# Optimization experiments

Measured on AMD Instinct MI355X. Metric: run time of the kernel, lower is better.

Reference implementation:

```python
import jax, jax.numpy as jnp
import numpy as np


def maxpool2x2(x):
    # NCHW 2x2 max pool, stride 2
    return jax.lax.reduce_window(x, -jnp.inf, jax.lax.max, (1, 1, 2, 2), (1, 1, 2, 2), 'VALID')


def _xavier_uniform(k, shape):
    fan_out, fan_in = shape
    lim = np.sqrt(6.0 / (fan_in + fan_out))
    return jax.random.uniform(k, shape, jnp.float32, -lim, lim)


def setup_inputs() -> dict:
    key = jax.random.key(0)
    ks = jax.random.split(key, 5)
    C = 64
    x = jax.random.normal(ks[0], (4, C, 128, 128), jnp.float32)
    Wq = _xavier_uniform(ks[1], (C // 8, C))  # 1x1 conv == channel matmul
    Wk = _xavier_uniform(ks[2], (C // 8, C))
    Wv = _xavier_uniform(ks[3], (C // 2, C))
    Wo = _xavier_uniform(ks[4], (C, C // 2))
    gamma = jnp.full((1,), 0.1, jnp.float32)  # nonzero so attention branch contributes
    return {"x": x, "Wq": Wq, "Wk": Wk, "Wv": Wv, "Wo": Wo, "gamma": gamma}


def reference(x, Wq, Wk, Wv, Wo, gamma):
    b, c, w, h = x.shape
    # 1x1 convs as channel contractions
    q = jnp.einsum('oc,bchw->bohw', Wq, x).reshape(b, c // 8, w * h)          # [b, c/8, k]
    k_ = maxpool2x2(jnp.einsum('oc,bchw->bohw', Wk, x)).reshape(b, c // 8, -1)  # [b, c/8, f]
    v = maxpool2x2(jnp.einsum('oc,bchw->bohw', Wv, x)).reshape(b, c // 2, -1)   # [b, c/2, f]
    # softmax over full-resolution query positions k (last axis), per pooled position f
    weights = jax.nn.softmax(jnp.einsum('bcf,bck->bfk', k_, q), axis=-1)        # [b, f, k]
    out = jnp.einsum('bcf,bfk->bck', v, weights).reshape(b, c // 2, w, h)       # [b, c/2, w, h]
    out = jnp.einsum('oc,bchw->bohw', Wo, out)                                   # [b, c, w, h]
    return gamma * out + x
```

## Files before the change

kernel.cpp:

```cpp
#include <hip/hip_runtime.h>
#include <cstdint>
#include <cstddef>


#define LOG2E 1.44269504088896340736f
#define FE_A 8388608.0f
#define FE_B 1064993098.0f

typedef __attribute__((ext_vector_type(8)))  __bf16 bf8_t;
typedef __attribute__((ext_vector_type(16))) float  fx16;

__device__ __forceinline__ unsigned short f2bf(float f) {
  unsigned int u = __builtin_bit_cast(unsigned int, f);
  u += 0x7FFFu + ((u >> 16) & 1u);
  return (unsigned short)(u >> 16);
}
__device__ __forceinline__ float bf2f(unsigned short h) {
  unsigned int u = ((unsigned int)h) << 16;
  return __builtin_bit_cast(float, u);
}
__device__ __forceinline__ unsigned int pk2(unsigned short lo, unsigned short hi) {
  return (unsigned int)lo | ((unsigned int)hi << 16);
}
__device__ __forceinline__ int pi16(int s) {
  int m = (s >> 2) & 3;
  return (m == 1 || m == 2) ? (s ^ 12) : s;
}
__device__ __forceinline__ unsigned fe_u(float s) {
  return (unsigned)fmaf(s, FE_A, FE_B);
}
__device__ __forceinline__ float fe_f(float s) {
  return __builtin_bit_cast(float, fe_u(s));
}
__device__ __forceinline__ unsigned fe_pk(float s0, float s1) {
  return __builtin_amdgcn_perm(fe_u(s1), fe_u(s0), 0x07060302);
}

#define MFMA __builtin_amdgcn_mfma_f32_32x32x16_bf16

__global__ void __launch_bounds__(256) k_qkv(const float* __restrict__ x,
                                             const float* __restrict__ Wq,
                                             const float* __restrict__ Wk,
                                             const float* __restrict__ Wv,
                                             const float* __restrict__ Wo,
                                             unsigned short* __restrict__ Qp,
                                             unsigned short* __restrict__ KpB,
                                             float* __restrict__ Vp,
                                             unsigned short* __restrict__ Wop) {
  if (blockIdx.x == 512) {
    for (int i = threadIdx.x; i < 2048; i += 256) {
      int c = i & 31;
      Wop[i] = f2bf(Wo[(i & ~31) | (c & 16) | pi16(c & 15)]);
    }
    return;
  }
  __shared__ unsigned int xs[128 * 64];
  int t = threadIdx.x;
  int b = blockIdx.x >> 7, rr = blockIdx.x & 127;
  int T = rr >> 1, ph = rr & 1;
  {
    int pos = t & 127, cslot = t >> 7;
    int r = pos >> 6, c = pos & 63;
    const float* xb =
        x + (size_t)b * (64 * 16384) + T * 256 + r * 128 + ph * 64 + c;
    int sw = pos & 15;
    unsigned int* row = xs + pos * 64;
#pragma unroll
    for (int i = 0; i < 16; ++i) {
      int p = cslot * 16 + i;
      float g0 = xb[(size_t)(2 * p) * 16384];
      float g1 = xb[(size_t)(2 * p + 1) * 16384];
      unsigned short h0 = f2bf(g0), h1 = f2bf(g1);
      unsigned short l0 = f2bf(g0 - bf2f(h0)), l1 = f2bf(g1 - bf2f(h1));
      int q = p >> 2, d = p & 3;
      row[((q + sw) & 15) * 4 + d] = pk2(h0, h1);
      row[((q + 8 + sw) & 15) * 4 + d] = pk2(l0, l1);
    }
  }
  int wv = t >> 6, lane = t & 63;
  int cg = wv & 1, Mt = wv >> 1;
  int m = lane & 31, h = lane >> 5;
  const float* wrow;
  float scale = 1.0f;
  bool zero = false;
  if (Mt == 0) {
    if (m < 8) wrow = Wq + m * 64;
    else if (m < 16) { wrow = Wk + (m - 8) * 64; scale = LOG2E; }
    else wrow = Wv + (m - 16) * 64;
  } else {
    if (m < 16) wrow = Wv + (m + 16) * 64;
    else { wrow = Wq; zero = true; }
  }
  bf8_t Ahi[4], Alo[4];
#pragma unroll
  for (int kk = 0; kk < 4; ++kk) {
    unsigned short hi8[8], lo8[8];
#pragma unroll
    for (int j = 0; j < 8; ++j) {
      float w = zero ? 0.f : wrow[kk * 16 + h * 8 + j] * scale;
      unsigned short wh = f2bf(w);
      hi8[j] = wh;
      lo8[j] = f2bf(w - bf2f(wh));
    }
    uint4 uh, ul;
    uh.x = pk2(hi8[0], hi8[1]); uh.y = pk2(hi8[2], hi8[3]);
    uh.z = pk2(hi8[4], hi8[5]); uh.w = pk2(hi8[6], hi8[7]);
    ul.x = pk2(lo8[0], lo8[1]); ul.y = pk2(lo8[2], lo8[3]);
    ul.z = pk2(lo8[4], lo8[5]); ul.w = pk2(lo8[6], lo8[7]);
    Ahi[kk] = __builtin_bit_cast(bf8_t, uh);
    Alo[kk] = __builtin_bit_cast(bf8_t, ul);
  }
  __syncthreads();
  fx16 z;
#pragma unroll
  for (int i = 0; i < 16; ++i) z[i] = 0.f;
  fx16 D0 = z, D1 = z;
#pragma unroll
  for (int r = 0; r < 2; ++r) {
    fx16 acc = z;
    int pos = r * 64 + cg * 32 + (lane & 31);
    const unsigned int* row = xs + pos * 64;
    int sw = pos & 15;
#pragma unroll
    for (int kk = 0; kk < 4; ++kk) {
      int q = 2 * kk + h;
      bf8_t Bh = *reinterpret_cast<const bf8_t*>(&row[((q + sw) & 15) * 4]);
      bf8_t Bl = *reinterpret_cast<const bf8_t*>(&row[((q + 8 + sw) & 15) * 4]);
      acc = MFMA(Ahi[kk], Bh, acc, 0, 0, 0);
      acc = MFMA(Ahi[kk], Bl, acc, 0, 0, 0);
      acc = MFMA(Alo[kk], Bh, acc, 0, 0, 0);
    }
    if (r == 0) D0 = acc; else D1 = acc;
  }
  uint2 z2; z2.x = z2.y = 0u;
  if (Mt == 0) {
#pragma unroll
    for (int r = 0; r < 2; ++r) {
      const fx16& D = r ? D1 : D0;
      int gpos = T * 256 + r * 128 + ph * 64 + cg * 32 + (lane & 31);
      unsigned short* qd = Qp + ((size_t)b * 16384 + gpos) * 16;
      uint2 qa;
      qa.x = pk2(f2bf(D[0]), f2bf(D[1]));
      qa.y = pk2(f2bf(D[2]), f2bf(D[3]));
      *reinterpret_cast<uint2*>(qd + h * 4) = qa;
      *reinterpret_cast<uint2*>(qd + 8 + h * 4) = z2;
    }
  }
  float pm[16];
#pragma unroll
  for (int r0 = 0; r0 < 16; ++r0) {
    float a = fmaxf(D0[r0], __shfl_xor(D0[r0], 1));
    float bb = fmaxf(D1[r0], __shfl_xor(D1[r0], 1));
    pm[r0] = fmaxf(a, bb);
  }
  if ((lane & 1) == 0) {
    int cell = ph * 32 + cg * 16 + ((lane & 31) >> 1);
    size_t idx = (size_t)b * 4096 + T * 64 + cell;
    float* vd = Vp + idx * 32;
    if (Mt == 0) {
      uint2 kw;
      kw.x = pk2(f2bf(pm[4]), f2bf(pm[5]));
      kw.y = pk2(f2bf(pm[6]), f2bf(pm[7]));
      *reinterpret_cast<uint2*>(KpB + idx * 16 + h * 4) = kw;
      *reinterpret_cast<float4*>(vd + h * 4) = make_float4(pm[8], pm[9], pm[10], pm[11]);
      *reinterpret_cast<float4*>(vd + 8 + h * 4) = make_float4(pm[12], pm[13], pm[14], pm[15]);
    } else {
      *reinterpret_cast<uint2*>(KpB + idx * 16 + 8 + h * 4) = z2;
      *reinterpret_cast<float4*>(vd + 16 + h * 4) = make_float4(pm[0], pm[1], pm[2], pm[3]);
      *reinterpret_cast<float4*>(vd + 24 + h * 4) = make_float4(pm[4], pm[5], pm[6], pm[7]);
    }
  }
}

__global__ void __launch_bounds__(64, 4) k_lsum(const unsigned short* __restrict__ Qp,
                                                const unsigned short* __restrict__ KpB,
                                                float* __restrict__ Lpart) {
  int b = blockIdx.x >> 10, gp = (blockIdx.x >> 4) & 63, ks = blockIdx.x & 15;
  int lane = threadIdx.x & 63;
  int half = lane >> 5, l31 = lane & 31;
  const unsigned short* kb =
      KpB + ((size_t)(b * 4096 + gp * 64 + l31)) * 16 + half * 8;
  bf8_t A0 = *reinterpret_cast<const bf8_t*>(kb);
  bf8_t A1 = *reinterpret_cast<const bf8_t*>(kb + 32 * 16);
  const unsigned short* qbase = Qp + ((size_t)b * 16384) * 16 + half * 8;
  fx16 z;
#pragma unroll
  for (int i = 0; i < 16; ++i) z[i] = 0.f;
  float l[32];
#pragma unroll
  for (int i = 0; i < 32; ++i) l[i] = 0.f;
  int t0 = ks * 32;
#define QLD(j) (*reinterpret_cast<const bf8_t*>( \
    qbase + (size_t)(((t0 + ((j) & 31)) * 32 + l31)) * 16))
  bf8_t Bc = QLD(0);
  fx16 sp0 = MFMA(A0, Bc, z, 0, 0, 0);
  fx16 sp1 = MFMA(A1, Bc, z, 0, 0, 0);
  Bc = QLD(1);
  bf8_t Bn = QLD(2);
  for (int i = 0; i < 32; ++i) {
    fx16 sn0 = MFMA(A0, Bc, z, 0, 0, 0);
    fx16 sn1 = MFMA(A1, Bc, z, 0, 0, 0);
#pragma unroll
    for (int r0 = 0; r0 < 16; ++r0) l[r0] += fe_f(sp0[r0]);
#pragma unroll
    for (int r0 = 0; r0 < 16; ++r0) l[16 + r0] += fe_f(sp1[r0]);
    sp0 = sn0; sp1 = sn1;
    Bc = Bn;
    Bn = QLD(i + 3);
  }
#undef QLD
#pragma unroll
  for (int r0 = 0; r0 < 32; ++r0)
    for (int d = 1; d < 32; d <<= 1) l[r0] += __shfl_xor(l[r0], d);
  if (l31 == 0) {
    size_t base = (size_t)ks * 16384 + b * 4096 + gp * 64;
#pragma unroll
    for (int r0 = 0; r0 < 16; ++r0) {
      int row = (r0 & 3) + 8 * (r0 >> 2) + 4 * half;
      Lpart[base + row] = l[r0];
      Lpart[base + 32 + row] = l[16 + r0];
    }
  }
}

__global__ void __launch_bounds__(256) k_pack(const float* __restrict__ Vp,
                                              const float* __restrict__ Lpart,
                                              unsigned short* __restrict__ Vpp) {
  int b = blockIdx.x >> 4, f0 = (blockIdx.x & 15) * 256;
  __shared__ unsigned short Tt[32][264];
  int t = threadIdx.x;
  size_t li = (size_t)b * 4096 + f0 + t;
  float L = 0.f;
#pragma unroll
  for (int p = 0; p < 16; ++p) L += Lpart[(size_t)p * 16384 + li];
  float rl = 1.0f / L;
  const float* vp = Vp + li * 32;
  int fl = (t & ~15) | pi16(t & 15);
  for (int c = 0; c < 32; ++c) Tt[c][fl] = f2bf(vp[c] * rl);
  __syncthreads();
  for (int u = t; u < 1024; u += 256) {
    int row = u >> 5, e0 = (u & 31) * 8;
    uint4 val = *reinterpret_cast<const uint4*>(&Tt[row][e0]);
    *reinterpret_cast<uint4*>(Vpp + ((size_t)b * 32 + row) * 4096 + f0 + e0) = val;
  }
}

__global__ void __launch_bounds__(256, 3) k_attn(const unsigned short* __restrict__ Qp,
                                                 const unsigned short* __restrict__ KpB,
                                                 const unsigned short* __restrict__ Vpp,
                                                 const unsigned short* __restrict__ Wop,
                                                 const float* __restrict__ x,
                                                 const float* __restrict__ gamma,
                                                 float* __restrict__ out) {
  int b = blockIdx.x >> 8, kp = blockIdx.x & 255;
  int wv = threadIdx.x >> 6, lane = threadIdx.x & 63;
  int half = lane >> 5, l31 = lane & 31;
  int kbase = kp * 64;
  const unsigned short* qb = Qp + ((size_t)b * 16384 + kbase + l31) * 16 + half * 8;
  bf8_t Bq0 = *reinterpret_cast<const bf8_t*>(qb);
  bf8_t Bq1 = *reinterpret_cast<const bf8_t*>(qb + 32 * 16);
  fx16 z;
#pragma unroll
  for (int i = 0; i < 16; ++i) z[i] = 0.f;
  fx16 acc0 = z, acc1 = z;
  const unsigned short* kpB = KpB + ((size_t)b * 4096 + l31) * 16 + half * 8;
  const unsigned short* vpB = Vpp + ((size_t)(b * 32 + l31)) * 4096 + half * 8;
  int c0 = wv * 32;
#define KLD(j) (*reinterpret_cast<const bf8_t*>(kpB + (size_t)((c0 + ((j) & 31)) * 32) * 16))
#define VLD(j, o) (*reinterpret_cast<const bf8_t*>(vpB + (c0 + ((j) & 31)) * 32 + (o)))
  bf8_t Akc = KLD(0);
  bf8_t Av0c = VLD(0, 0), Av1c = VLD(0, 16);
  fx16 sp0 = MFMA(Akc, Bq0, z, 0, 0, 0);
  fx16 sp1 = MFMA(Akc, Bq1, z, 0, 0, 0);
  Akc = KLD(1);
  bf8_t Av0n = VLD(1, 0), Av1n = VLD(1, 16);
  bf8_t Akin = KLD(2);
  for (int fc = 0; fc < 32; ++fc) {
    fx16 sn0 = MFMA(Akc, Bq0, z, 0, 0, 0);
    uint4 u00, u01;
    u00.x = fe_pk(sp0[0], sp0[1]);   u00.y = fe_pk(sp0[2], sp0[3]);
    u00.z = fe_pk(sp0[4], sp0[5]);   u00.w = fe_pk(sp0[6], sp0[7]);
    u01.x = fe_pk(sp0[8], sp0[9]);   u01.y = fe_pk(sp0[10], sp0[11]);
    u01.z = fe_pk(sp0[12], sp0[13]); u01.w = fe_pk(sp0[14], sp0[15]);
    acc0 = MFMA(Av0c, __builtin_bit_cast(bf8_t, u00), acc0, 0, 0, 0);
    acc0 = MFMA(Av1c, __builtin_bit_cast(bf8_t, u01), acc0, 0, 0, 0);
    fx16 sn1 = MFMA(Akc, Bq1, z, 0, 0, 0);
    uint4 u10, u11;
    u10.x = fe_pk(sp1[0], sp1[1]);   u10.y = fe_pk(sp1[2], sp1[3]);
    u10.z = fe_pk(sp1[4], sp1[5]);   u10.w = fe_pk(sp1[6], sp1[7]);
    u11.x = fe_pk(sp1[8], sp1[9]);   u11.y = fe_pk(sp1[10], sp1[11]);
    u11.z = fe_pk(sp1[12], sp1[13]); u11.w = fe_pk(sp1[14], sp1[15]);
    acc1 = MFMA(Av0c, __builtin_bit_cast(bf8_t, u10), acc1, 0, 0, 0);
    acc1 = MFMA(Av1c, __builtin_bit_cast(bf8_t, u11), acc1, 0, 0, 0);
    sp0 = sn0; sp1 = sn1;
    Akc = Akin; Av0c = Av0n; Av1c = Av1n;
    Akin = KLD(fc + 3);
    Av0n = VLD(fc + 2, 0); Av1n = VLD(fc + 2, 16);
  }
#undef KLD
#undef VLD
  __shared__ float sacc[4][2][4][64][4];
#pragma unroll
  for (int j4 = 0; j4 < 4; ++j4) {
    *reinterpret_cast<float4*>(&sacc[wv][0][j4][lane][0]) =
        make_float4(acc0[4 * j4], acc0[4 * j4 + 1], acc0[4 * j4 + 2], acc0[4 * j4 + 3]);
    *reinterpret_cast<float4*>(&sacc[wv][1][j4][lane][0]) =
        make_float4(acc1[4 * j4], acc1[4 * j4 + 1], acc1[4 * j4 + 2], acc1[4 * j4 + 3]);
  }
  __syncthreads();
  if (wv >= 2) return;
  int kt = wv;
  int k = kbase + kt * 32 + l31;
  const float* xp = x + (size_t)b * 64 * 16384 + k;
  float xv0[16], xv1[16];
#pragma unroll
  for (int r0 = 0; r0 < 16; ++r0) {
    int row = (r0 & 3) + 8 * (r0 >> 2) + 4 * half;
    xv0[r0] = xp[(size_t)row * 16384];
    xv1[r0] = xp[(size_t)(row + 32) * 16384];
  }
  fx16 tot;
#pragma unroll
  for (int j4 = 0; j4 < 4; ++j4) {
    float4 a0 = *reinterpret_cast<const float4*>(&sacc[0][kt][j4][lane][0]);
    float4 a1 = *reinterpret_cast<const float4*>(&sacc[1][kt][j4][lane][0]);
    float4 a2 = *reinterpret_cast<const float4*>(&sacc[2][kt][j4][lane][0]);
    float4 a3 = *reinterpret_cast<const float4*>(&sacc[3][kt][j4][lane][0]);
    tot[4 * j4]     = (a0.x + a1.x) + (a2.x + a3.x);
    tot[4 * j4 + 1] = (a0.y + a1.y) + (a2.y + a3.y);
    tot[4 * j4 + 2] = (a0.z + a1.z) + (a2.z + a3.z);
    tot[4 * j4 + 3] = (a0.w + a1.w) + (a2.w + a3.w);
  }
  bf8_t Ob0, Ob1;
#pragma unroll
  for (int j = 0; j < 8; ++j) { Ob0[j] = (__bf16)tot[j]; Ob1[j] = (__bf16)tot[8 + j]; }
  const unsigned short* wb = Wop + l31 * 32 + half * 8;
  bf8_t Aw00 = *reinterpret_cast<const bf8_t*>(wb);
  bf8_t Aw01 = *reinterpret_cast<const bf8_t*>(wb + 16);
  bf8_t Aw10 = *reinterpret_cast<const bf8_t*>(wb + 1024);
  bf8_t Aw11 = *reinterpret_cast<const bf8_t*>(wb + 1024 + 16);
  fx16 y0 = MFMA(Aw00, Ob0, z, 0, 0, 0);
  y0 = MFMA(Aw01, Ob1, y0, 0, 0, 0);
  fx16 y1 = MFMA(Aw10, Ob0, z, 0, 0, 0);
  y1 = MFMA(Aw11, Ob1, y1, 0, 0, 0);
  float g = gamma[0];
  float* op = out + (size_t)b * 64 * 16384 + k;
#pragma unroll
  for (int r0 = 0; r0 < 16; ++r0) {
    int row = (r0 & 3) + 8 * (r0 >> 2) + 4 * half;
    op[(size_t)row * 16384]        = fmaf(g, y0[r0], xv0[r0]);
    op[(size_t)(row + 32) * 16384] = fmaf(g, y1[r0], xv1[r0]);
  }
}

extern "C" void kernel_launch(void* const* d_in, const int* in_sizes, int n_in,
                              void* d_out, int out_size, void* d_ws, size_t ws_size,
                              hipStream_t stream) {
  const float* x     = (const float*)d_in[0];
  const float* Wq    = (const float*)d_in[1];
  const float* Wk    = (const float*)d_in[2];
  const float* Wv    = (const float*)d_in[3];
  const float* Wo    = (const float*)d_in[4];
  const float* gamma = (const float*)d_in[5];
  float* out = (float*)d_out;
  char* ws = (char*)d_ws;
  unsigned short* Qp    = (unsigned short*)(ws + 0);
  unsigned short* KpB   = (unsigned short*)(ws + 2097152);
  float*          Vp    = (float*)(ws + 2621440);
  unsigned short* Vpp   = (unsigned short*)(ws + 4718592);
  float*          Lpart = (float*)(ws + 5767168);
  unsigned short* Wop   = (unsigned short*)(ws + 6815744);

  k_qkv <<<dim3(513),  dim3(256), 0, stream>>>(x, Wq, Wk, Wv, Wo, Qp, KpB, Vp, Wop);
  k_lsum<<<dim3(4096), dim3(64),  0, stream>>>(Qp, KpB, Lpart);
  k_pack<<<dim3(64),   dim3(256), 0, stream>>>(Vp, Lpart, Vpp);
  k_attn<<<dim3(1024), dim3(256), 0, stream>>>(Qp, KpB, Vpp, Wop, x, gamma, out);
}
```

Before: 157.4 us.

## Repartition lsum and pack kernels, add explicit MFMA/exp interleaving schedules

k_lsum now gives each 64-lane wave one 32-row key tile over a 32-tile query slice, with two waves per block. This doubles the wave count and halves per-wave register state. It unrolls by two with sched_group_barrier hints so MFMA, loads and exp VALU work interleave. k_pack uses 256 smaller blocks with vectorized float4 loads, and k_attn's main loop is unrolled into even/odd halves with similar scheduling hints. The aim is more parallelism and better latency hiding; the risks are the scheduler constraints hurting codegen and Lpart slice indexing needing to stay consistent.

```diff
diff --git a/kernel.cpp b/kernel.cpp
--- a/kernel.cpp
+++ b/kernel.cpp
@@ -9,6 +9,12 @@
 
 typedef __attribute__((ext_vector_type(8)))  __bf16 bf8_t;
 typedef __attribute__((ext_vector_type(16))) float  fx16;
+
+#if __has_builtin(__builtin_amdgcn_sched_group_barrier)
+#define SGB(m, n) __builtin_amdgcn_sched_group_barrier(m, n, 0)
+#else
+#define SGB(m, n)
+#endif
 
 __device__ __forceinline__ unsigned short f2bf(float f) {
   unsigned int u = __builtin_bit_cast(unsigned int, f);
@@ -172,53 +178,53 @@
   }
 }
 
-__global__ void __launch_bounds__(64, 4) k_lsum(const unsigned short* __restrict__ Qp,
-                                                const unsigned short* __restrict__ KpB,
-                                                float* __restrict__ Lpart) {
-  int b = blockIdx.x >> 10, gp = (blockIdx.x >> 4) & 63, ks = blockIdx.x & 15;
-  int lane = threadIdx.x & 63;
+__global__ void __launch_bounds__(128, 4) k_lsum(const unsigned short* __restrict__ Qp,
+                                                 const unsigned short* __restrict__ KpB,
+                                                 float* __restrict__ Lpart) {
+  int b = blockIdx.x >> 10;
+  int r = blockIdx.x & 1023;
+  int fg = r >> 3, ks = r & 7;
+  int wv = threadIdx.x >> 6, lane = threadIdx.x & 63;
   int half = lane >> 5, l31 = lane & 31;
-  const unsigned short* kb =
-      KpB + ((size_t)(b * 4096 + gp * 64 + l31)) * 16 + half * 8;
-  bf8_t A0 = *reinterpret_cast<const bf8_t*>(kb);
-  bf8_t A1 = *reinterpret_cast<const bf8_t*>(kb + 32 * 16);
+  int slice = ks * 2 + wv;
+  bf8_t A = *reinterpret_cast<const bf8_t*>(
+      KpB + ((size_t)(b * 4096 + fg * 32 + l31)) * 16 + half * 8);
   const unsigned short* qbase = Qp + ((size_t)b * 16384) * 16 + half * 8;
   fx16 z;
 #pragma unroll
   for (int i = 0; i < 16; ++i) z[i] = 0.f;
-  float l[32];
-#pragma unroll
-  for (int i = 0; i < 32; ++i) l[i] = 0.f;
-  int t0 = ks * 32;
+  float l[16];
+#pragma unroll
+  for (int i = 0; i < 16; ++i) l[i] = 0.f;
+  int t0 = slice * 32;
 #define QLD(j) (*reinterpret_cast<const bf8_t*>( \
     qbase + (size_t)(((t0 + ((j) & 31)) * 32 + l31)) * 16))
-  bf8_t Bc = QLD(0);
-  fx16 sp0 = MFMA(A0, Bc, z, 0, 0, 0);
-  fx16 sp1 = MFMA(A1, Bc, z, 0, 0, 0);
-  Bc = QLD(1);
-  bf8_t Bn = QLD(2);
-  for (int i = 0; i < 32; ++i) {
-    fx16 sn0 = MFMA(A0, Bc, z, 0, 0, 0);
-    fx16 sn1 = MFMA(A1, Bc, z, 0, 0, 0);
-#pragma unroll
-    for (int r0 = 0; r0 < 16; ++r0) l[r0] += fe_f(sp0[r0]);
-#pragma unroll
-    for (int r0 = 0; r0 < 16; ++r0) l[16 + r0] += fe_f(sp1[r0]);
-    sp0 = sn0; sp1 = sn1;
-    Bc = Bn;
-    Bn = QLD(i + 3);
+  bf8_t BqE = QLD(0);
+  fx16 sE = MFMA(A, BqE, z, 0, 0, 0);
+  bf8_t BqO = QLD(1);
+  for (int it = 0; it < 16; ++it) {
+    int e = 2 * it;
+    fx16 sO = MFMA(A, BqO, z, 0, 0, 0);
+    BqE = QLD(e + 2);
+#pragma unroll
+    for (int r0 = 0; r0 < 16; ++r0) l[r0] += fe_f(sE[r0]);
+    SGB(0x8, 1); SGB(0x20, 1); SGB(0x2, 48);
+    sE = MFMA(A, BqE, z, 0, 0, 0);
+    BqO = QLD(e + 3);
+#pragma unroll
+    for (int r0 = 0; r0 < 16; ++r0) l[r0] += fe_f(sO[r0]);
+    SGB(0x8, 1); SGB(0x20, 1); SGB(0x2, 48);
   }
 #undef QLD
 #pragma unroll
-  for (int r0 = 0; r0 < 32; ++r0)
+  for (int r0 = 0; r0 < 16; ++r0)
     for (int d = 1; d < 32; d <<= 1) l[r0] += __shfl_xor(l[r0], d);
   if (l31 == 0) {
-    size_t base = (size_t)ks * 16384 + b * 4096 + gp * 64;
+    size_t base = (size_t)slice * 16384 + b * 4096 + fg * 32;
 #pragma unroll
     for (int r0 = 0; r0 < 16; ++r0) {
       int row = (r0 & 3) + 8 * (r0 >> 2) + 4 * half;
       Lpart[base + row] = l[r0];
-      Lpart[base + 32 + row] = l[16 + r0];
     }
   }
 }
@@ -226,23 +232,31 @@
 __global__ void __launch_bounds__(256) k_pack(const float* __restrict__ Vp,
                                               const float* __restrict__ Lpart,
                                               unsigned short* __restrict__ Vpp) {
-  int b = blockIdx.x >> 4, f0 = (blockIdx.x & 15) * 256;
-  __shared__ unsigned short Tt[32][264];
+  int b = blockIdx.x >> 6, f0 = (blockIdx.x & 63) * 64;
+  __shared__ unsigned short Tt[32][72];
   int t = threadIdx.x;
-  size_t li = (size_t)b * 4096 + f0 + t;
+  int floc = t & 63, cq = t >> 6;
+  size_t li = (size_t)b * 4096 + f0 + floc;
   float L = 0.f;
 #pragma unroll
   for (int p = 0; p < 16; ++p) L += Lpart[(size_t)p * 16384 + li];
   float rl = 1.0f / L;
-  const float* vp = Vp + li * 32;
-  int fl = (t & ~15) | pi16(t & 15);
-  for (int c = 0; c < 32; ++c) Tt[c][fl] = f2bf(vp[c] * rl);
+  const float* vp = Vp + li * 32 + cq * 8;
+  float4 v0 = *reinterpret_cast<const float4*>(vp);
+  float4 v1 = *reinterpret_cast<const float4*>(vp + 4);
+  int fl = (floc & ~15) | pi16(floc & 15);
+  Tt[cq * 8 + 0][fl] = f2bf(v0.x * rl);
+  Tt[cq * 8 + 1][fl] = f2bf(v0.y * rl);
+  Tt[cq * 8 + 2][fl] = f2bf(v0.z * rl);
+  Tt[cq * 8 + 3][fl] = f2bf(v0.w * rl);
+  Tt[cq * 8 + 4][fl] = f2bf(v1.x * rl);
+  Tt[cq * 8 + 5][fl] = f2bf(v1.y * rl);
+  Tt[cq * 8 + 6][fl] = f2bf(v1.z * rl);
+  Tt[cq * 8 + 7][fl] = f2bf(v1.w * rl);
   __syncthreads();
-  for (int u = t; u < 1024; u += 256) {
-    int row = u >> 5, e0 = (u & 31) * 8;
-    uint4 val = *reinterpret_cast<const uint4*>(&Tt[row][e0]);
-    *reinterpret_cast<uint4*>(Vpp + ((size_t)b * 32 + row) * 4096 + f0 + e0) = val;
-  }
+  int row = t >> 3, seg = t & 7;
+  uint4 val = *reinterpret_cast<const uint4*>(&Tt[row][seg * 8]);
+  *reinterpret_cast<uint4*>(Vpp + ((size_t)b * 32 + row) * 4096 + f0 + seg * 8) = val;
 }
 
 __global__ void __launch_bounds__(256, 3) k_attn(const unsigned short* __restrict__ Qp,
@@ -268,34 +282,53 @@
   int c0 = wv * 32;
 #define KLD(j) (*reinterpret_cast<const bf8_t*>(kpB + (size_t)((c0 + ((j) & 31)) * 32) * 16))
 #define VLD(j, o) (*reinterpret_cast<const bf8_t*>(vpB + (c0 + ((j) & 31)) * 32 + (o)))
-  bf8_t Akc = KLD(0);
-  bf8_t Av0c = VLD(0, 0), Av1c = VLD(0, 16);
-  fx16 sp0 = MFMA(Akc, Bq0, z, 0, 0, 0);
-  fx16 sp1 = MFMA(Akc, Bq1, z, 0, 0, 0);
-  Akc = KLD(1);
-  bf8_t Av0n = VLD(1, 0), Av1n = VLD(1, 16);
-  bf8_t Akin = KLD(2);
-  for (int fc = 0; fc < 32; ++fc) {
-    fx16 sn0 = MFMA(Akc, Bq0, z, 0, 0, 0);
-    uint4 u00, u01;
-    u00.x = fe_pk(sp0[0], sp0[1]);   u00.y = fe_pk(sp0[2], sp0[3]);
-    u00.z = fe_pk(sp0[4], sp0[5]);   u00.w = fe_pk(sp0[6], sp0[7]);
-    u01.x = fe_pk(sp0[8], sp0[9]);   u01.y = fe_pk(sp0[10], sp0[11]);
-    u01.z = fe_pk(sp0[12], sp0[13]); u01.w = fe_pk(sp0[14], sp0[15]);
-    acc0 = MFMA(Av0c, __builtin_bit_cast(bf8_t, u00), acc0, 0, 0, 0);
-    acc0 = MFMA(Av1c, __builtin_bit_cast(bf8_t, u01), acc0, 0, 0, 0);
-    fx16 sn1 = MFMA(Akc, Bq1, z, 0, 0, 0);
-    uint4 u10, u11;
-    u10.x = fe_pk(sp1[0], sp1[1]);   u10.y = fe_pk(sp1[2], sp1[3]);
-    u10.z = fe_pk(sp1[4], sp1[5]);   u10.w = fe_pk(sp1[6], sp1[7]);
-    u11.x = fe_pk(sp1[8], sp1[9]);   u11.y = fe_pk(sp1[10], sp1[11]);
-    u11.z = fe_pk(sp1[12], sp1[13]); u11.w = fe_pk(sp1[14], sp1[15]);
-    acc1 = MFMA(Av0c, __builtin_bit_cast(bf8_t, u10), acc1, 0, 0, 0);
-    acc1 = MFMA(Av1c, __builtin_bit_cast(bf8_t, u11), acc1, 0, 0, 0);
-    sp0 = sn0; sp1 = sn1;
-    Akc = Akin; Av0c = Av0n; Av1c = Av1n;
-    Akin = KLD(fc + 3);
-    Av0n = VLD(fc + 2, 0); Av1n = VLD(fc + 2, 16);
+  bf8_t Ak0 = KLD(0);
+  bf8_t VE0 = VLD(0, 0), VE1 = VLD(0, 16);
+  fx16 sE0 = MFMA(Ak0, Bq0, z, 0, 0, 0);
+  fx16 sE1 = MFMA(Ak0, Bq1, z, 0, 0, 0);
+  bf8_t AkO = KLD(1);
+  for (int it = 0; it < 16; ++it) {
+    int e = 2 * it;
+    fx16 sO0 = MFMA(AkO, Bq0, z, 0, 0, 0);
+    fx16 sO1 = MFMA(AkO, Bq1, z, 0, 0, 0);
+    bf8_t VO0 = VLD(e + 1, 0), VO1 = VLD(e + 1, 16);
+    bf8_t AkE = KLD(e + 2);
+    {
+      uint4 u00, u01, u10, u11;
+      u00.x = fe_pk(sE0[0], sE0[1]);   u00.y = fe_pk(sE0[2], sE0[3]);
+      u00.z = fe_pk(sE0[4], sE0[5]);   u00.w = fe_pk(sE0[6], sE0[7]);
+      u01.x = fe_pk(sE0[8], sE0[9]);   u01.y = fe_pk(sE0[10], sE0[11]);
+      u01.z = fe_pk(sE0[12], sE0[13]); u01.w = fe_pk(sE0[14], sE0[15]);
+      u10.x = fe_pk(sE1[0], sE1[1]);   u10.y = fe_pk(sE1[2], sE1[3]);
+      u10.z = fe_pk(sE1[4], sE1[5]);   u10.w = fe_pk(sE1[6], sE1[7]);
+      u11.x = fe_pk(sE1[8], sE1[9]);   u11.y = fe_pk(sE1[10], sE1[11]);
+      u11.z = fe_pk(sE1[12], sE1[13]); u11.w = fe_pk(sE1[14], sE1[15]);
+      acc0 = MFMA(VE0, __builtin_bit_cast(bf8_t, u00), acc0, 0, 0, 0);
+      acc0 = MFMA(VE1, __builtin_bit_cast(bf8_t, u01), acc0, 0, 0, 0);
+      acc1 = MFMA(VE0, __builtin_bit_cast(bf8_t, u10), acc1, 0, 0, 0);
+      acc1 = MFMA(VE1, __builtin_bit_cast(bf8_t, u11), acc1, 0, 0, 0);
+    }
+    SGB(0x8, 2); SGB(0x20, 3); SGB(0x2, 80); SGB(0x8, 4);
+    sE0 = MFMA(AkE, Bq0, z, 0, 0, 0);
+    sE1 = MFMA(AkE, Bq1, z, 0, 0, 0);
+    VE0 = VLD(e + 2, 0); VE1 = VLD(e + 2, 16);
+    AkO = KLD(e + 3);
+    {
+      uint4 u00, u01, u10, u11;
+      u00.x = fe_pk(sO0[0], sO0[1]);   u00.y = fe_pk(sO0[2], sO0[3]);
+      u00.z = fe_pk(sO0[4], sO0[5]);   u00.w = fe_pk(sO0[6], sO0[7]);
+      u01.x = fe_pk(sO0[8], sO0[9]);   u01.y = fe_pk(sO0[10], sO0[11]);
+      u01.z = fe_pk(sO0[12], sO0[13]); u01.w = fe_pk(sO0[14], sO0[15]);
+      u10.x = fe_pk(sO1[0], sO1[1]);   u10.y = fe_pk(sO1[2], sO1[3]);
+      u10.z = fe_pk(sO1[4], sO1[5]);   u10.w = fe_pk(sO1[6], sO1[7]);
+      u11.x = fe_pk(sO1[8], sO1[9]);   u11.y = fe_pk(sO1[10], sO1[11]);
+      u11.z = fe_pk(sO1[12], sO1[13]); u11.w = fe_pk(sO1[14], sO1[15]);
+      acc0 = MFMA(VO0, __builtin_bit_cast(bf8_t, u00), acc0, 0, 0, 0);
+      acc0 = MFMA(VO1, __builtin_bit_cast(bf8_t, u01), acc0, 0, 0, 0);
+      acc1 = MFMA(VO0, __builtin_bit_cast(bf8_t, u10), acc1, 0, 0, 0);
+      acc1 = MFMA(VO1, __builtin_bit_cast(bf8_t, u11), acc1, 0, 0, 0);
+    }
+    SGB(0x8, 2); SGB(0x20, 3); SGB(0x2, 80); SGB(0x8, 4);
   }
 #undef KLD
 #undef VLD
@@ -372,7 +405,7 @@
   unsigned short* Wop   = (unsigned short*)(ws + 6815744);
 
   k_qkv <<<dim3(513),  dim3(256), 0, stream>>>(x, Wq, Wk, Wv, Wo, Qp, KpB, Vp, Wop);
-  k_lsum<<<dim3(4096), dim3(64),  0, stream>>>(Qp, KpB, Lpart);
-  k_pack<<<dim3(64),   dim3(256), 0, stream>>>(Vp, Lpart, Vpp);
+  k_lsum<<<dim3(4096), dim3(128), 0, stream>>>(Qp, KpB, Lpart);
+  k_pack<<<dim3(256),  dim3(256), 0, stream>>>(Vp, Lpart, Vpp);
   k_attn<<<dim3(1024), dim3(256), 0, stream>>>(Qp, KpB, Vpp, Wop, x, gamma, out);
 }
```

After: 152.0 us. 3.4% less time.
